# Performance work log

Hardware: AMD Instinct MI355X
Metric: run time of the kernel (lower is better)

Reference implementation:

```python
import jax, jax.numpy as jnp
import numpy as np
import math

B, N, L, ED, H = 2, 32, 4, 64, 4   # graphs, nodes/graph, layers, embed_dim, heads
HD = ED // H
EPS = 1e-5


def _ln(x, g, b):
    m = x.mean(-1, keepdims=True)
    v = ((x - m) ** 2).mean(-1, keepdims=True)
    return (x - m) * jax.lax.rsqrt(v + EPS) * g + b


def _layer(x, W, b, lg, lb, fW, fb, fg, fbeta):
    # NOTE: in the torch source, ModuleList([Linear]*4) shares ONE linear for
    # q/k/v1/v2 and ONE LayerNorm for norms[0..2]; we reproduce that sharing.
    h = (x @ W.T + b).reshape(B, N, N, H, HD)
    q = _ln(h, lg, lb)                                    # q == k (shared LN)
    scores = jnp.einsum('bxahd,bayhd->bxayh', q, q) / math.sqrt(HD)
    att = jax.nn.softmax(scores, axis=2)                  # softmax over 'a'
    xu = jnp.einsum('bxahd,bayhd->bxayhd', h, h)          # v1 == v2 == h
    xu = _ln(xu, lg, lb)                                  # shared LN again
    xu = jnp.einsum('bxayh,bxayhd->bxyhd', att, xu).reshape(B, N, N, ED)
    y = jnp.concatenate([x, xu], axis=-1) @ fW.T + fb
    return _ln(y, fg, fbeta)


def _diag_offdiag_maxpool(x):
    # x: (B, ED, N, N)
    diag = jnp.diagonal(x, axis1=-2, axis2=-1)            # (B, ED, N)
    max_diag = diag.max(axis=2)                           # (B, ED)
    val = jnp.abs(max_diag.max() + (-x).max())
    eye = jnp.eye(N, dtype=x.dtype)
    max_offdiag = (x - val * eye).max(axis=(2, 3))        # (B, ED)
    return jnp.concatenate([max_diag, max_offdiag], axis=1)  # (B, 2*ED)


def setup_inputs() -> dict:
    key = jax.random.key(0)
    ks = jax.random.split(key, 12)
    E = 1024
    g = jax.random.randint(ks[0], (E,), 0, B)
    ls = jax.random.randint(ks[1], (E,), 0, N)
    ld = jax.random.randint(ks[2], (E,), 0, N)
    edge_index = jnp.stack([g * N + ls, g * N + ld]).astype(jnp.int64)
    batch = (jnp.arange(B * N) // N).astype(jnp.int64)
    std = 0.02
    return {
        'edge_index': edge_index,
        'batch': batch,
        'W0': jax.random.normal(ks[3], (ED, 1), jnp.float32) * std,
        'b0': jnp.zeros((ED,), jnp.float32),
        'Ws': jax.random.normal(ks[4], (L - 1, ED, ED), jnp.float32) * std,
        'bs': jnp.zeros((L - 1, ED), jnp.float32),
        'ln_g': jnp.ones((L, HD), jnp.float32),
        'ln_b': jnp.zeros((L, HD), jnp.float32),
        'fW0': jax.random.normal(ks[5], (ED, 1 + ED), jnp.float32) * std,
        'fb0': jnp.zeros((ED,), jnp.float32),
        'fWs': jax.random.normal(ks[6], (L - 1, ED, 2 * ED), jnp.float32) * std,
        'fbs': jnp.zeros((L - 1, ED), jnp.float32),
        'fln_g': jnp.ones((L, ED), jnp.float32),
        'fln_b': jnp.zeros((L, ED), jnp.float32),
        'opW': jax.random.normal(ks[7], (L, ED // 2, 2 * ED), jnp.float32) * std,
        'opb': jnp.zeros((L, ED // 2), jnp.float32),
    }


def reference(edge_index, batch, W0, b0, Ws, bs, ln_g, ln_b,
              fW0, fb0, fWs, fbs, fln_g, fln_b, opW, opb):
    # to_dense_adj with edge_attr = 1.0
    g = batch[edge_index[0]]
    ls = edge_index[0] - g * N
    ld = edge_index[1] - g * N
    adj = jnp.zeros((B, N, N), jnp.float32).at[g, ls, ld].add(1.0)
    idx = jnp.arange(N)
    adj = adj.at[:, idx, idx].set(2.0)
    x = adj[..., None]                                    # (B, N, N, 1)

    scores = jnp.zeros((B, ED // 2), jnp.float32)
    for i in range(L):
        W = W0 if i == 0 else Ws[i - 1]
        b = b0 if i == 0 else bs[i - 1]
        fW = fW0 if i == 0 else fWs[i - 1]
        fb = fb0 if i == 0 else fbs[i - 1]
        x = _layer(x, W, b, ln_g[i], ln_b[i], fW, fb, fln_g[i], fln_b[i])
        pooled = _diag_offdiag_maxpool(jnp.transpose(x, (0, 3, 1, 2)))
        scores = scores + pooled @ opW[i].T + opb[i]

    # BatchNorm1d(momentum=1.0, affine=False), training mode -> batch stats
    m = scores.mean(axis=0)
    v = scores.var(axis=0)
    return (scores - m) / jnp.sqrt(v + EPS)
```

## Files before the change

kernel.cpp:

```cpp
#include <hip/hip_runtime.h>
#include <math.h>

#define EPS 1e-5f

#define AG_LOAD(p)     __hip_atomic_load((p), __ATOMIC_RELAXED, __HIP_MEMORY_SCOPE_AGENT)
#define AG_STORE(p, v) __hip_atomic_store((p), (v), __ATOMIC_RELAXED, __HIP_MEMORY_SCOPE_AGENT)

struct Params {
    const int* ei; const int* batch; int E;
    const float* W0; const float* b0; const float* Ws; const float* bs;
    const float* ln_g; const float* ln_b;
    const float* fW0; const float* fb0; const float* fWs; const float* fbs;
    const float* fln_g; const float* fln_b;
    const float* opW; const float* opb;
    float* hA; float* hAT;
    float* hB; float* hBT;
    float* xbuf;
    float* Pmin; float* Poff; float* Pdg;
    int* bar;
    float* out;
};

__launch_bounds__(512, 1)
__global__ void k0(Params p) {
    const int tid  = threadIdx.x;
    const int blk  = blockIdx.x;
    const int gtid = blk * 512 + tid;
    const int c    = tid & 63;
    const int d    = c & 15;
    const int rl   = tid >> 6;
    const int r0     = blk * 8;
    const int b_blk  = r0 >> 10;
    const int xi_blk = (r0 >> 5) & 31;
    const int y0     = r0 & 31;
    const int rld    = xi_blk - y0;
    const int a_l  = c & 31;
    const int h1   = c >> 5;

    __shared__ float xslab[32];
    __shared__ float yslab[256];
    __shared__ __align__(16) float cA[64], cC[64], cW[64], cB0[64], cG[64], cBl[64];
    __shared__ float hstat[3][4];
    __shared__ __align__(16) float pp_s[256 * 68];
    __shared__ float A1_s[8 * 132];
    __shared__ float K0h_s[8][4];
    __shared__ __align__(16) float xrow[8][64];
    __shared__ __align__(16) float xu_s[8][64];
    __shared__ float Wf0[64];
    __shared__ __align__(16) float T65[64 * 68];
    __shared__ __align__(16) float ST[64 * 68];

    if (blk == 0 && tid == 0) p.bar[0] = 0;

    if (tid < 32)  xslab[tid] = 0.0f;
    if (tid < 256) yslab[tid] = 0.0f;

    if (tid < 64) {
        float Wc = p.W0[c], bc = p.b0[c];
        float sW = Wc, sB = bc;
        #pragma unroll
        for (int m = 1; m < 16; m <<= 1) {
            sW += __shfl_xor(sW, m, 16);
            sB += __shfl_xor(sB, m, 16);
        }
        float Ac = Wc - sW * 0.0625f;
        float Bc = bc - sB * 0.0625f;
        float sAA = Ac * Ac, sAB = Ac * Bc, sBB = Bc * Bc;
        #pragma unroll
        for (int m = 1; m < 16; m <<= 1) {
            sAA += __shfl_xor(sAA, m, 16);
            sAB += __shfl_xor(sAB, m, 16);
            sBB += __shfl_xor(sBB, m, 16);
        }
        cA[c] = Ac; cC[c] = Bc; cW[c] = Wc; cB0[c] = bc;
        cG[c] = p.ln_g[d]; cBl[c] = p.ln_b[d];
        if (d == 0) {
            hstat[0][c >> 4] = sAA * 0.0625f;
            hstat[1][c >> 4] = sAB * 0.0625f;
            hstat[2][c >> 4] = sBB * 0.0625f;
        }
        Wf0[tid] = p.fW0[tid * 65];
    }
    for (int i = tid; i < 1024; i += 512) {
        int cc = i >> 4, u = i & 15;
        const float* src = p.fW0 + cc * 65 + 1 + 4 * u;
        float4 w = make_float4(src[0], src[1], src[2], src[3]);
        *(float4*)(T65 + cc * 68 + 4 * ((u + 2 * cc) & 15)) = w;
    }
    for (int i = tid; i < 1024; i += 512) {
        float4 w = ((const float4*)p.Ws)[i];
        int cc = i >> 4, u = i & 15;
        *(float4*)(ST + cc * 68 + 4 * ((u + 2 * cc) & 15)) = w;
    }
    __syncthreads();

    for (int e2 = tid; e2 < p.E; e2 += 512) {
        int e0 = p.ei[e2], e1 = p.ei[p.E + e2];
        int g  = p.batch[e0];
        if (g == b_blk) {
            int ls = e0 - g * 32, ld = e1 - g * 32;
            if (ls == xi_blk) atomicAdd(&xslab[ld], 1.0f);
            unsigned dy = (unsigned)(ld - y0);
            if (dy < 8u) atomicAdd(&yslab[ls * 8 + dy], 1.0f);
        }
    }
    __syncthreads();
    if (tid == 0) xslab[xi_blk] = 2.0f;
    if (tid < 8)  yslab[(y0 + tid) * 8 + tid] = 2.0f;
    __syncthreads();

    const float vx = xslab[a_l];
    const float vy = yslab[a_l * 8 + rl];
    float s0, s1, is0, is1, w0m, w1m;
    {
        const int hh = h1;
        float rsx = rsqrtf(fmaf(fmaf(hstat[0][hh], vx, 2.0f * hstat[1][hh]), vx, hstat[2][hh]) + EPS);
        float rsy = rsqrtf(fmaf(fmaf(hstat[0][hh], vy, 2.0f * hstat[1][hh]), vy, hstat[2][hh]) + EPS);
        float qq = 0.f, sp = 0.f, sq = 0.f;
        #pragma unroll
        for (int t = 0; t < 4; ++t) {
            int dd = hh * 16 + 4 * t;
            float4 av = *(const float4*)(cA + dd);
            float4 bv = *(const float4*)(cC + dd);
            float4 wv = *(const float4*)(cW + dd);
            float4 b0v = *(const float4*)(cB0 + dd);
            float4 gv = *(const float4*)(cG + dd);
            float4 blv = *(const float4*)(cBl + dd);
            float4 ppv;
            float qx, qy;
            qx = fmaf(av.x, vx, bv.x) * rsx * gv.x + blv.x;
            qy = fmaf(av.x, vy, bv.x) * rsy * gv.x + blv.x;
            qq = fmaf(qx, qy, qq);
            ppv.x = fmaf(wv.x, vx, b0v.x) * fmaf(wv.x, vy, b0v.x);
            qx = fmaf(av.y, vx, bv.y) * rsx * gv.y + blv.y;
            qy = fmaf(av.y, vy, bv.y) * rsy * gv.y + blv.y;
            qq = fmaf(qx, qy, qq);
            ppv.y = fmaf(wv.y, vx, b0v.y) * fmaf(wv.y, vy, b0v.y);
            qx = fmaf(av.z, vx, bv.z) * rsx * gv.z + blv.z;
            qy = fmaf(av.z, vy, bv.z) * rsy * gv.z + blv.z;
            qq = fmaf(qx, qy, qq);
            ppv.z = fmaf(wv.z, vx, b0v.z) * fmaf(wv.z, vy, b0v.z);
            qx = fmaf(av.w, vx, bv.w) * rsx * gv.w + blv.w;
            qy = fmaf(av.w, vy, bv.w) * rsy * gv.w + blv.w;
            qq = fmaf(qx, qy, qq);
            ppv.w = fmaf(wv.w, vx, b0v.w) * fmaf(wv.w, vy, b0v.w);
            sp += ppv.x + ppv.y + ppv.z + ppv.w;
            sq += ppv.x*ppv.x + ppv.y*ppv.y + ppv.z*ppv.z + ppv.w*ppv.w;
            *(float4*)(pp_s + (a_l * 8 + rl) * 68 + 4 * (((hh * 4 + t) + 3 * a_l) & 15)) = ppv;
        }
        s0 = qq * 0.25f;
        float mu = sp * 0.0625f, var = fmaxf(sq * 0.0625f - mu * mu, 0.f);
        is0 = rsqrtf(var + EPS); w0m = mu * is0;
    }
    {
        const int hh = h1 + 2;
        float rsx = rsqrtf(fmaf(fmaf(hstat[0][hh], vx, 2.0f * hstat[1][hh]), vx, hstat[2][hh]) + EPS);
        float rsy = rsqrtf(fmaf(fmaf(hstat[0][hh], vy, 2.0f * hstat[1][hh]), vy, hstat[2][hh]) + EPS);
        float qq = 0.f, sp = 0.f, sq = 0.f;
        #pragma unroll
        for (int t = 0; t < 4; ++t) {
            int dd = hh * 16 + 4 * t;
            float4 av = *(const float4*)(cA + dd);
            float4 bv = *(const float4*)(cC + dd);
            float4 wv = *(const float4*)(cW + dd);
            float4 b0v = *(const float4*)(cB0 + dd);
            float4 gv = *(const float4*)(cG + dd);
            float4 blv = *(const float4*)(cBl + dd);
            float4 ppv;
            float qx, qy;
            qx = fmaf(av.x, vx, bv.x) * rsx * gv.x + blv.x;
            qy = fmaf(av.x, vy, bv.x) * rsy * gv.x + blv.x;
            qq = fmaf(qx, qy, qq);
            ppv.x = fmaf(wv.x, vx, b0v.x) * fmaf(wv.x, vy, b0v.x);
            qx = fmaf(av.y, vx, bv.y) * rsx * gv.y + blv.y;
            qy = fmaf(av.y, vy, bv.y) * rsy * gv.y + blv.y;
            qq = fmaf(qx, qy, qq);
            ppv.y = fmaf(wv.y, vx, b0v.y) * fmaf(wv.y, vy, b0v.y);
            qx = fmaf(av.z, vx, bv.z) * rsx * gv.z + blv.z;
            qy = fmaf(av.z, vy, bv.z) * rsy * gv.z + blv.z;
            qq = fmaf(qx, qy, qq);
            ppv.z = fmaf(wv.z, vx, b0v.z) * fmaf(wv.z, vy, b0v.z);
            qx = fmaf(av.w, vx, bv.w) * rsx * gv.w + blv.w;
            qy = fmaf(av.w, vy, bv.w) * rsy * gv.w + blv.w;
            qq = fmaf(qx, qy, qq);
            ppv.w = fmaf(wv.w, vx, b0v.w) * fmaf(wv.w, vy, b0v.w);
            sp += ppv.x + ppv.y + ppv.z + ppv.w;
            sq += ppv.x*ppv.x + ppv.y*ppv.y + ppv.z*ppv.z + ppv.w*ppv.w;
            *(float4*)(pp_s + (a_l * 8 + rl) * 68 + 4 * (((hh * 4 + t) + 3 * a_l) & 15)) = ppv;
        }
        s1 = qq * 0.25f;
        float mu = sp * 0.0625f, var = fmaxf(sq * 0.0625f - mu * mu, 0.f);
        is1 = rsqrtf(var + EPS); w1m = mu * is1;
    }

    float m0 = s0, m1 = s1;
    #pragma unroll
    for (int m = 1; m < 32; m <<= 1) {
        m0 = fmaxf(m0, __shfl_xor(m0, m));
        m1 = fmaxf(m1, __shfl_xor(m1, m));
    }
    float e0 = __expf(s0 - m0), e1 = __expf(s1 - m1);
    float l0 = e0, l1 = e1, k0a = e0 * w0m, k1a = e1 * w1m;
    #pragma unroll
    for (int m = 1; m < 32; m <<= 1) {
        l0 += __shfl_xor(l0, m);  l1 += __shfl_xor(l1, m);
        k0a += __shfl_xor(k0a, m); k1a += __shfl_xor(k1a, m);
    }
    A1_s[rl * 132 + h1 * 33 + a_l]       = e0 * is0 / l0;
    A1_s[rl * 132 + (h1 + 2) * 33 + a_l] = e1 * is1 / l1;
    if (a_l == 0) {
        K0h_s[rl][h1]     = k0a / l0;
        K0h_s[rl][h1 + 2] = k1a / l1;
    }

    {
        const int hc = c >> 4;
        float acc = 0.f;
        #pragma unroll
        for (int a = 0; a < 32; ++a) {
            float pv = pp_s[(a * 8 + rl) * 68 + 4 * (((c >> 2) + 3 * a) & 15) + (c & 3)];
            acc = fmaf(A1_s[rl * 132 + hc * 33 + a], pv, acc);
        }
        xu_s[rl][c] = (acc - K0h_s[rl][hc]) * cG[c] + cBl[c];
    }

    const float adjv = xslab[y0 + rl];
    float acc2 = fmaf(Wf0[c], adjv, p.fb0[c]);
    #pragma unroll
    for (int u = 0; u < 16; ++u) {
        float4 w = *(const float4*)(T65 + c * 68 + 4 * ((u + 2 * c) & 15));
        float4 xr = *(const float4*)(&xu_s[rl][4 * u]);
        acc2 = fmaf(w.x, xr.x, acc2); acc2 = fmaf(w.y, xr.y, acc2);
        acc2 = fmaf(w.z, xr.z, acc2); acc2 = fmaf(w.w, xr.w, acc2);
    }
    float t1 = acc2;
    #pragma unroll
    for (int m = 1; m < 64; m <<= 1) t1 += __shfl_xor(t1, m, 64);
    float mu = t1 * (1.0f / 64.0f);
    float dv2 = acc2 - mu;
    float t2 = dv2 * dv2;
    #pragma unroll
    for (int m = 1; m < 64; m <<= 1) t2 += __shfl_xor(t2, m, 64);
    float xnew = dv2 * rsqrtf(t2 * (1.0f / 64.0f) + EPS) * p.fln_g[c] + p.fln_b[c];
    xrow[rl][c]  = xnew;
    p.xbuf[gtid] = xnew;
    __syncthreads();

    if (tid < 64) {
        float mn = 1e30f, off = -1e30f, dg = -1e30f;
        #pragma unroll
        for (int r2 = 0; r2 < 8; ++r2) {
            float v = xrow[r2][tid];
            mn = fminf(mn, v);
            if (r2 == rld) dg = v; else off = fmaxf(off, v);
        }
        int o = blk * 64 + tid;
        p.Pmin[o] = mn; p.Poff[o] = off; p.Pdg[o] = dg;
    }

    {
        float acc = p.bs[c];
        #pragma unroll
        for (int u = 0; u < 16; ++u) {
            float4 w = *(const float4*)(ST + c * 68 + 4 * ((u + 2 * c) & 15));
            float4 xr = *(const float4*)(&xrow[rl][4 * u]);
            acc = fmaf(w.x, xr.x, acc); acc = fmaf(w.y, xr.y, acc);
            acc = fmaf(w.z, xr.z, acc); acc = fmaf(w.w, xr.w, acc);
        }
        p.hA[gtid] = acc;
        p.hAT[((b_blk * 32 + y0 + rl) * 32 + xi_blk) * 64 + c] = acc;
    }
}

__launch_bounds__(512, 1)
__global__ void klayer(Params p, int layer, int is_last) {
    const int tid  = threadIdx.x;
    const int blk  = blockIdx.x;
    const int gtid = blk * 512 + tid;
    const int c    = tid & 63;
    const int d    = c & 15;
    const int rl   = tid >> 6;
    const int r0     = blk * 8;
    const int b_blk  = r0 >> 10;
    const int xi_blk = (r0 >> 5) & 31;
    const int y0     = r0 & 31;
    const int rld    = xi_blk - y0;
    const int slab_off = (b_blk * 1024 + xi_blk * 32) * 64;
    const int a_l  = c & 31;
    const int h1   = c >> 5;

    const float* hin  = (layer == 2) ? p.hB  : p.hA;
    const float* hinT = (layer == 2) ? p.hBT : p.hAT;
    float* hout  = (layer == 1) ? p.hB  : p.hA;
    float* houtT = (layer == 1) ? p.hBT : p.hAT;

    __shared__ __align__(16) float hx_s[32 * 68];
    __shared__ __align__(16) float yT_s[256 * 68];
    __shared__ float A1_s[8 * 132];
    __shared__ float K0h_s[8][4];
    __shared__ __align__(16) float xrow[8][64];
    __shared__ __align__(16) float xu_s[8][64];
    __shared__ __align__(16) float FT[64 * 132];
    __shared__ __align__(16) float ST[64 * 68];
    __shared__ __align__(16) float g16[16], b16[16];
    __shared__ float vals[4];
    __shared__ float scores_s[64];
    __shared__ int tailflag;
    float* sm_mn  = yT_s;
    float* sm_off = yT_s + 512;
    float* sm_dg  = yT_s + 1024;
    float* psum   = yT_s + 1536;

    float xv = p.xbuf[gtid];
    {
        const float4* src = (const float4*)(hinT + (b_blk * 32 + y0) * 2048);
        #pragma unroll
        for (int k = 0; k < 8; ++k) {
            int i = tid + k * 512;
            float4 v = src[i];
            int rl2 = i >> 9, a = (i >> 4) & 31, u = i & 15;
            *(float4*)(yT_s + (rl2 * 32 + a) * 68 + 4 * ((u + 2 * a) & 15)) = v;
        }
    }
    {
        float4 hsl = ((const float4*)(hin + slab_off))[tid];
        int a = tid >> 4, t = tid & 15, pr = (t + 2 * a) & 15;
        *(float4*)(hx_s + a * 68 + 4 * pr) = hsl;
    }
    if (tid < 16) {
        g16[tid] = p.ln_g[layer * 16 + tid];
        b16[tid] = p.ln_b[layer * 16 + tid];
    }
    {
        const float* fw = p.fWs + (layer - 1) * 8192;
        for (int i = tid; i < 2048; i += 512) {
            float4 w = ((const float4*)fw)[i];
            int cc = i >> 5, u = i & 31;
            *(float4*)(FT + cc * 132 + 4 * ((u + 2 * cc) & 31)) = w;
        }
    }
    if (!is_last) {
        const float* sw = p.Ws + layer * 4096;
        for (int i = tid; i < 1024; i += 512) {
            float4 w = ((const float4*)sw)[i];
            int cc = i >> 4, u = i & 15;
            *(float4*)(ST + cc * 68 + 4 * ((u + 2 * cc) & 15)) = w;
        }
    }
    xrow[rl][c] = xv;
    __syncthreads();

    float s0, s1, is0, is1, w0m, w1m;
    {
        const int hh = h1;
        float4 xh4[4], yh4[4];
        float sxp = 0.f, sxq = 0.f, syp = 0.f, syq = 0.f;
        #pragma unroll
        for (int t = 0; t < 4; ++t) {
            int ps = 4 * (((hh * 4 + t) + 2 * a_l) & 15);
            float4 v = *(const float4*)(hx_s + a_l * 68 + ps);
            float4 y = *(const float4*)(yT_s + (rl * 32 + a_l) * 68 + ps);
            xh4[t] = v; yh4[t] = y;
            sxp += v.x + v.y + v.z + v.w;
            sxq += v.x*v.x + v.y*v.y + v.z*v.z + v.w*v.w;
            syp += y.x + y.y + y.z + y.w;
            syq += y.x*y.x + y.y*y.y + y.z*y.z + y.w*y.w;
        }
        float mxm = sxp * 0.0625f;
        float rsx = rsqrtf(fmaxf(sxq * 0.0625f - mxm * mxm, 0.f) + EPS);
        float mym = syp * 0.0625f;
        float rsy = rsqrtf(fmaxf(syq * 0.0625f - mym * mym, 0.f) + EPS);
        float qq = 0.f, sp = 0.f, sq = 0.f;
        #pragma unroll
        for (int t = 0; t < 4; ++t) {
            float4 g4 = *(const float4*)(g16 + 4 * t);
            float4 b4 = *(const float4*)(b16 + 4 * t);
            float4 xh = xh4[t], yh = yh4[t];
            float4 ppv;
            float qx, qy;
            qx = (xh.x - mxm) * rsx * g4.x + b4.x;
            qy = (yh.x - mym) * rsy * g4.x + b4.x;
            qq = fmaf(qx, qy, qq);  ppv.x = xh.x * yh.x;
            qx = (xh.y - mxm) * rsx * g4.y + b4.y;
            qy = (yh.y - mym) * rsy * g4.y + b4.y;
            qq = fmaf(qx, qy, qq);  ppv.y = xh.y * yh.y;
            qx = (xh.z - mxm) * rsx * g4.z + b4.z;
            qy = (yh.z - mym) * rsy * g4.z + b4.z;
            qq = fmaf(qx, qy, qq);  ppv.z = xh.z * yh.z;
            qx = (xh.w - mxm) * rsx * g4.w + b4.w;
            qy = (yh.w - mym) * rsy * g4.w + b4.w;
            qq = fmaf(qx, qy, qq);  ppv.w = xh.w * yh.w;
            sp += ppv.x + ppv.y + ppv.z + ppv.w;
            sq += ppv.x*ppv.x + ppv.y*ppv.y + ppv.z*ppv.z + ppv.w*ppv.w;
        }
        s0 = qq * 0.25f;
        float mu = sp * 0.0625f, var = fmaxf(sq * 0.0625f - mu * mu, 0.f);
        is0 = rsqrtf(var + EPS); w0m = mu * is0;
    }
    {
        const int hh = h1 + 2;
        float4 xh4[4], yh4[4];
        float sxp = 0.f, sxq = 0.f, syp = 0.f, syq = 0.f;
        #pragma unroll
        for (int t = 0; t < 4; ++t) {
            int ps = 4 * (((hh * 4 + t) + 2 * a_l) & 15);
            float4 v = *(const float4*)(hx_s + a_l * 68 + ps);
            float4 y = *(const float4*)(yT_s + (rl * 32 + a_l) * 68 + ps);
            xh4[t] = v; yh4[t] = y;
            sxp += v.x + v.y + v.z + v.w;
            sxq += v.x*v.x + v.y*v.y + v.z*v.z + v.w*v.w;
            syp += y.x + y.y + y.z + y.w;
            syq += y.x*y.x + y.y*y.y + y.z*y.z + y.w*y.w;
        }
        float mxm = sxp * 0.0625f;
        float rsx = rsqrtf(fmaxf(sxq * 0.0625f - mxm * mxm, 0.f) + EPS);
        float mym = syp * 0.0625f;
        float rsy = rsqrtf(fmaxf(syq * 0.0625f - mym * mym, 0.f) + EPS);
        float qq = 0.f, sp = 0.f, sq = 0.f;
        #pragma unroll
        for (int t = 0; t < 4; ++t) {
            float4 g4 = *(const float4*)(g16 + 4 * t);
            float4 b4 = *(const float4*)(b16 + 4 * t);
            float4 xh = xh4[t], yh = yh4[t];
            float4 ppv;
            float qx, qy;
            qx = (xh.x - mxm) * rsx * g4.x + b4.x;
            qy = (yh.x - mym) * rsy * g4.x + b4.x;
            qq = fmaf(qx, qy, qq);  ppv.x = xh.x * yh.x;
            qx = (xh.y - mxm) * rsx * g4.y + b4.y;
            qy = (yh.y - mym) * rsy * g4.y + b4.y;
            qq = fmaf(qx, qy, qq);  ppv.y = xh.y * yh.y;
            qx = (xh.z - mxm) * rsx * g4.z + b4.z;
            qy = (yh.z - mym) * rsy * g4.z + b4.z;
            qq = fmaf(qx, qy, qq);  ppv.z = xh.z * yh.z;
            qx = (xh.w - mxm) * rsx * g4.w + b4.w;
            qy = (yh.w - mym) * rsy * g4.w + b4.w;
            qq = fmaf(qx, qy, qq);  ppv.w = xh.w * yh.w;
            sp += ppv.x + ppv.y + ppv.z + ppv.w;
            sq += ppv.x*ppv.x + ppv.y*ppv.y + ppv.z*ppv.z + ppv.w*ppv.w;
        }
        s1 = qq * 0.25f;
        float mu = sp * 0.0625f, var = fmaxf(sq * 0.0625f - mu * mu, 0.f);
        is1 = rsqrtf(var + EPS); w1m = mu * is1;
    }

    float m0 = s0, m1 = s1;
    #pragma unroll
    for (int m = 1; m < 32; m <<= 1) {
        m0 = fmaxf(m0, __shfl_xor(m0, m));
        m1 = fmaxf(m1, __shfl_xor(m1, m));
    }
    float e0 = __expf(s0 - m0), e1 = __expf(s1 - m1);
    float l0 = e0, l1 = e1, k0a = e0 * w0m, k1a = e1 * w1m;
    #pragma unroll
    for (int m = 1; m < 32; m <<= 1) {
        l0 += __shfl_xor(l0, m);  l1 += __shfl_xor(l1, m);
        k0a += __shfl_xor(k0a, m); k1a += __shfl_xor(k1a, m);
    }
    A1_s[rl * 132 + h1 * 33 + a_l]       = e0 * is0 / l0;
    A1_s[rl * 132 + (h1 + 2) * 33 + a_l] = e1 * is1 / l1;
    if (a_l == 0) {
        K0h_s[rl][h1]     = k0a / l0;
        K0h_s[rl][h1 + 2] = k1a / l1;
    }

    {
        const int hc = c >> 4;
        const int ce = c & 3;
        float acc = 0.f;
        #pragma unroll
        for (int a = 0; a < 32; ++a) {
            int ps = 4 * (((c >> 2) + 2 * a) & 15) + ce;
            float hxv = hx_s[a * 68 + ps];
            float hyv = yT_s[(rl * 32 + a) * 68 + ps];
            acc = fmaf(A1_s[rl * 132 + hc * 33 + a], hxv * hyv, acc);
        }
        xu_s[rl][c] = (acc - K0h_s[rl][hc]) * g16[d] + b16[d];
    }

    float acc2 = p.fbs[(layer - 1) * 64 + c];
    #pragma unroll
    for (int u = 0; u < 16; ++u) {
        float4 w = *(const float4*)(FT + c * 132 + 4 * ((u + 2 * c) & 31));
        float4 xr = *(const float4*)(&xrow[rl][4 * u]);
        acc2 = fmaf(w.x, xr.x, acc2); acc2 = fmaf(w.y, xr.y, acc2);
        acc2 = fmaf(w.z, xr.z, acc2); acc2 = fmaf(w.w, xr.w, acc2);
    }
    #pragma unroll
    for (int u = 16; u < 32; ++u) {
        float4 w = *(const float4*)(FT + c * 132 + 4 * ((u + 2 * c) & 31));
        float4 xr = *(const float4*)(&xu_s[rl][4 * (u - 16)]);
        acc2 = fmaf(w.x, xr.x, acc2); acc2 = fmaf(w.y, xr.y, acc2);
        acc2 = fmaf(w.z, xr.z, acc2); acc2 = fmaf(w.w, xr.w, acc2);
    }
    float t1 = acc2;
    #pragma unroll
    for (int m = 1; m < 64; m <<= 1) t1 += __shfl_xor(t1, m, 64);
    float mu = t1 * (1.0f / 64.0f);
    float dv2 = acc2 - mu;
    float t2 = dv2 * dv2;
    #pragma unroll
    for (int m = 1; m < 64; m <<= 1) t2 += __shfl_xor(t2, m, 64);
    float xnew = dv2 * rsqrtf(t2 * (1.0f / 64.0f) + EPS) *
                 p.fln_g[layer * 64 + c] + p.fln_b[layer * 64 + c];
    __syncthreads();
    xrow[rl][c] = xnew;
    if (!is_last) p.xbuf[gtid] = xnew;
    __syncthreads();

    if (tid < 64) {
        float mn = 1e30f, off = -1e30f, dg = -1e30f;
        #pragma unroll
        for (int r2 = 0; r2 < 8; ++r2) {
            float v = xrow[r2][tid];
            mn = fminf(mn, v);
            if (r2 == rld) dg = v; else off = fmaxf(off, v);
        }
        int o = layer * 16384 + blk * 64 + tid;
        if (is_last) {
            AG_STORE(&p.Pmin[o], mn); AG_STORE(&p.Poff[o], off); AG_STORE(&p.Pdg[o], dg);
        } else {
            p.Pmin[o] = mn; p.Poff[o] = off; p.Pdg[o] = dg;
        }
    }

    if (!is_last) {
        float acc = p.bs[layer * 64 + c];
        #pragma unroll
        for (int u = 0; u < 16; ++u) {
            float4 w = *(const float4*)(ST + c * 68 + 4 * ((u + 2 * c) & 15));
            float4 xr = *(const float4*)(&xrow[rl][4 * u]);
            acc = fmaf(w.x, xr.x, acc); acc = fmaf(w.y, xr.y, acc);
            acc = fmaf(w.z, xr.z, acc); acc = fmaf(w.w, xr.w, acc);
        }
        hout[gtid] = acc;
        houtT[((b_blk * 32 + y0 + rl) * 32 + xi_blk) * 64 + c] = acc;
        return;
    }

    __syncthreads();
    if (tid == 0) {
        int r = __hip_atomic_fetch_add(p.bar, 1, __ATOMIC_RELAXED,
                                       __HIP_MEMORY_SCOPE_AGENT);
        tailflag = (r == 255) ? 1 : 0;
    }
    __syncthreads();
    if (!tailflag) return;

    {
        int l = tid >> 7, bb = (tid >> 6) & 1, e = tid & 63;
        float mn = 1e30f, off = -1e30f, dg = -1e30f;
        #pragma unroll 4
        for (int k = 0; k < 128; ++k) {
            int o = l * 16384 + (bb * 128 + k) * 64 + e;
            float vmn, voff, vdg;
            if (l == 3) { vmn = AG_LOAD(&p.Pmin[o]); voff = AG_LOAD(&p.Poff[o]); vdg = AG_LOAD(&p.Pdg[o]); }
            else        { vmn = p.Pmin[o];           voff = p.Poff[o];           vdg = p.Pdg[o]; }
            mn  = fminf(mn,  vmn);
            off = fmaxf(off, voff);
            dg  = fmaxf(dg,  vdg);
        }
        sm_mn[tid] = mn; sm_off[tid] = off; sm_dg[tid] = dg;
    }
    __syncthreads();
    if (tid < 4) {
        float gmx = -1e30f, gmn = 1e30f;
        for (int i2 = 0; i2 < 128; ++i2) {
            gmx = fmaxf(gmx, sm_dg[tid * 128 + i2]);
            gmn = fminf(gmn, sm_mn[tid * 128 + i2]);
        }
        vals[tid] = fabsf(gmx - gmn);
    }
    __syncthreads();
    {
        int bb = tid >> 8, cc = (tid >> 3) & 31, pp = tid & 7;
        float a2 = 0.0f;
        for (int l = 0; l < 4; ++l) {
            float val = vals[l];
            const float* Wr = p.opW + l * 4096 + cc * 128;
            int base = l * 128 + bb * 64;
            for (int j = pp * 16; j < pp * 16 + 16; ++j) {
                float pv;
                if (j < 64) pv = sm_dg[base + j];
                else        pv = fmaxf(sm_off[base + j - 64], sm_dg[base + j - 64] - val);
                a2 = fmaf(Wr[j], pv, a2);
            }
        }
        psum[tid] = a2;
    }
    __syncthreads();
    if (tid < 64) {
        int bb = tid >> 5, cc = tid & 31;
        float a2 = 0.0f;
        for (int l = 0; l < 4; ++l) a2 += p.opb[l * 32 + cc];
        for (int pp = 0; pp < 8; ++pp) a2 += psum[bb * 256 + cc * 8 + pp];
        scores_s[tid] = a2;
    }
    __syncthreads();
    if (tid < 32) {
        float sA = scores_s[tid], sB = scores_s[32 + tid];
        float mu2 = 0.5f * (sA + sB);
        float va = 0.5f * ((sA - mu2) * (sA - mu2) + (sB - mu2) * (sB - mu2));
        float inv = rsqrtf(va + EPS);
        p.out[tid]      = (sA - mu2) * inv;
        p.out[32 + tid] = (sB - mu2) * inv;
    }
}

extern "C" void kernel_launch(void* const* d_in, const int* in_sizes, int n_in,
                              void* d_out, int out_size, void* d_ws, size_t ws_size,
                              hipStream_t stream) {
    Params prm;
    prm.ei    = (const int*)d_in[0];
    prm.batch = (const int*)d_in[1];
    prm.E     = in_sizes[0] / 2;
    prm.W0    = (const float*)d_in[2];
    prm.b0    = (const float*)d_in[3];
    prm.Ws    = (const float*)d_in[4];
    prm.bs    = (const float*)d_in[5];
    prm.ln_g  = (const float*)d_in[6];
    prm.ln_b  = (const float*)d_in[7];
    prm.fW0   = (const float*)d_in[8];
    prm.fb0   = (const float*)d_in[9];
    prm.fWs   = (const float*)d_in[10];
    prm.fbs   = (const float*)d_in[11];
    prm.fln_g = (const float*)d_in[12];
    prm.fln_b = (const float*)d_in[13];
    prm.opW   = (const float*)d_in[14];
    prm.opb   = (const float*)d_in[15];

    float* ws = (float*)d_ws;
    prm.hA    = ws;
    prm.hAT   = prm.hA   + 131072;
    prm.hB    = prm.hAT  + 131072;
    prm.hBT   = prm.hB   + 131072;
    prm.xbuf  = prm.hBT  + 131072;
    prm.Pmin  = prm.xbuf + 131072;
    prm.Poff  = prm.Pmin + 65536;
    prm.Pdg   = prm.Poff + 65536;
    prm.bar   = (int*)(prm.Pdg + 65536);
    prm.out   = (float*)d_out;

    k0<<<256, 512, 0, stream>>>(prm);
    klayer<<<256, 512, 0, stream>>>(prm, 1, 0);
    klayer<<<256, 512, 0, stream>>>(prm, 2, 0);
    klayer<<<256, 512, 0, stream>>>(prm, 3, 1);
}
```

Baseline: 157.5 us.

## Retile to 2x2 row blocks with 512 workgroups and atomic order-preserving pooling

Each workgroup now handles a 2x2 tile of (x,y) positions, where it used to handle a row of 8. That means 256-thread blocks, 512 blocks and two blocks per CU, with two x-slabs and two y-slabs staged in shared memory. Per-block pooling partials are replaced by global atomicMax on order-preserving encoded floats into a small 512-entry buffer, which is zeroed by a memset. The tail block then reads only that buffer and no longer reduces 64K partials. The pp_s buffer is dropped and products are recomputed, and the Ws staging reuses the FT buffer. Smaller shared memory improves occupancy, but each slab is loaded more redundantly and there are more atomics plus an extra memset launch.

```diff
diff --git a/kernel.cpp b/kernel.cpp
--- a/kernel.cpp
+++ b/kernel.cpp
@@ -4,7 +4,15 @@
 #define EPS 1e-5f
 
 #define AG_LOAD(p)     __hip_atomic_load((p), __ATOMIC_RELAXED, __HIP_MEMORY_SCOPE_AGENT)
-#define AG_STORE(p, v) __hip_atomic_store((p), (v), __ATOMIC_RELAXED, __HIP_MEMORY_SCOPE_AGENT)
+
+__device__ __forceinline__ unsigned fenc(float f) {
+    unsigned u = __float_as_uint(f);
+    return (u & 0x80000000u) ? ~u : (u | 0x80000000u);
+}
+__device__ __forceinline__ float fdec(unsigned u) {
+    u = (u & 0x80000000u) ? (u & 0x7FFFFFFFu) : ~u;
+    return __uint_as_float(u);
+}
 
 struct Params {
     const int* ei; const int* batch; int E;
@@ -16,44 +24,50 @@
     float* hA; float* hAT;
     float* hB; float* hBT;
     float* xbuf;
-    float* Pmin; float* Poff; float* Pdg;
+    unsigned* PdgU; unsigned* PoffU; unsigned* PmnU;
     int* bar;
     float* out;
 };
 
-__launch_bounds__(512, 1)
+
+__device__ __forceinline__ void pool_atomic(Params& p, int layer, int b_blk, int e,
+                                            float mn, float off, float dg) {
+    int o = layer * 128 + b_blk * 64 + e;
+    atomicMax(&p.PdgU[o],  fenc(dg));
+    atomicMax(&p.PoffU[o], fenc(off));
+    atomicMax(&p.PmnU[o],  fenc(-mn));
+}
+
+__launch_bounds__(256, 2)
 __global__ void k0(Params p) {
     const int tid  = threadIdx.x;
     const int blk  = blockIdx.x;
-    const int gtid = blk * 512 + tid;
+    const int gtid = blk * 256 + tid;
     const int c    = tid & 63;
     const int d    = c & 15;
     const int rl   = tid >> 6;
-    const int r0     = blk * 8;
-    const int b_blk  = r0 >> 10;
-    const int xi_blk = (r0 >> 5) & 31;
-    const int y0     = r0 & 31;
-    const int rld    = xi_blk - y0;
+    const int rx   = rl >> 1;
+    const int ry   = rl & 1;
+    const int b_blk = blk >> 8;
+    const int x0    = ((blk >> 4) & 15) * 2;
+    const int y0    = (blk & 15) * 2;
     const int a_l  = c & 31;
     const int h1   = c >> 5;
 
-    __shared__ float xslab[32];
-    __shared__ float yslab[256];
+    __shared__ float xslab2[2 * 32];
+    __shared__ float yslab2[32 * 2];
     __shared__ __align__(16) float cA[64], cC[64], cW[64], cB0[64], cG[64], cBl[64];
     __shared__ float hstat[3][4];
-    __shared__ __align__(16) float pp_s[256 * 68];
-    __shared__ float A1_s[8 * 132];
-    __shared__ float K0h_s[8][4];
-    __shared__ __align__(16) float xrow[8][64];
-    __shared__ __align__(16) float xu_s[8][64];
+    __shared__ float A1_s[4 * 132];
+    __shared__ float K0h_s[4][4];
+    __shared__ __align__(16) float xrow[4][64];
+    __shared__ __align__(16) float xu_s[4][64];
     __shared__ float Wf0[64];
     __shared__ __align__(16) float T65[64 * 68];
     __shared__ __align__(16) float ST[64 * 68];
 
-    if (blk == 0 && tid == 0) p.bar[0] = 0;
-
-    if (tid < 32)  xslab[tid] = 0.0f;
-    if (tid < 256) yslab[tid] = 0.0f;
+    if (tid < 64)  xslab2[tid] = 0.0f;
+    if (tid >= 64 && tid < 128) yslab2[tid - 64] = 0.0f;
 
     if (tid < 64) {
         float Wc = p.W0[c], bc = p.b0[c];
@@ -81,39 +95,45 @@
         }
         Wf0[tid] = p.fW0[tid * 65];
     }
-    for (int i = tid; i < 1024; i += 512) {
+    #pragma unroll
+    for (int s = 0; s < 4; ++s) {
+        int i = tid + s * 256;
         int cc = i >> 4, u = i & 15;
         const float* src = p.fW0 + cc * 65 + 1 + 4 * u;
         float4 w = make_float4(src[0], src[1], src[2], src[3]);
         *(float4*)(T65 + cc * 68 + 4 * ((u + 2 * cc) & 15)) = w;
     }
-    for (int i = tid; i < 1024; i += 512) {
+    #pragma unroll
+    for (int s = 0; s < 4; ++s) {
+        int i = tid + s * 256;
         float4 w = ((const float4*)p.Ws)[i];
         int cc = i >> 4, u = i & 15;
         *(float4*)(ST + cc * 68 + 4 * ((u + 2 * cc) & 15)) = w;
     }
     __syncthreads();
 
-    for (int e2 = tid; e2 < p.E; e2 += 512) {
+    for (int e2 = tid; e2 < p.E; e2 += 256) {
         int e0 = p.ei[e2], e1 = p.ei[p.E + e2];
         int g  = p.batch[e0];
         if (g == b_blk) {
             int ls = e0 - g * 32, ld = e1 - g * 32;
-            if (ls == xi_blk) atomicAdd(&xslab[ld], 1.0f);
+            unsigned dx = (unsigned)(ls - x0);
+            if (dx < 2u) atomicAdd(&xslab2[dx * 32 + ld], 1.0f);
             unsigned dy = (unsigned)(ld - y0);
-            if (dy < 8u) atomicAdd(&yslab[ls * 8 + dy], 1.0f);
-        }
-    }
-    __syncthreads();
-    if (tid == 0) xslab[xi_blk] = 2.0f;
-    if (tid < 8)  yslab[(y0 + tid) * 8 + tid] = 2.0f;
-    __syncthreads();
-
-    const float vx = xslab[a_l];
-    const float vy = yslab[a_l * 8 + rl];
+            if (dy < 2u) atomicAdd(&yslab2[ls * 2 + dy], 1.0f);
+        }
+    }
+    __syncthreads();
+    if (tid < 2)  xslab2[tid * 32 + x0 + tid] = 2.0f;
+    if (tid >= 2 && tid < 4) { int j = tid - 2; yslab2[(y0 + j) * 2 + j] = 2.0f; }
+    __syncthreads();
+
+    const float vx = xslab2[rx * 32 + a_l];
+    const float vy = yslab2[a_l * 2 + ry];
     float s0, s1, is0, is1, w0m, w1m;
-    {
-        const int hh = h1;
+    #pragma unroll
+    for (int hb = 0; hb < 2; ++hb) {
+        const int hh = h1 + 2 * hb;
         float rsx = rsqrtf(fmaf(fmaf(hstat[0][hh], vx, 2.0f * hstat[1][hh]), vx, hstat[2][hh]) + EPS);
         float rsy = rsqrtf(fmaf(fmaf(hstat[0][hh], vy, 2.0f * hstat[1][hh]), vy, hstat[2][hh]) + EPS);
         float qq = 0.f, sp = 0.f, sq = 0.f;
@@ -126,71 +146,29 @@
             float4 b0v = *(const float4*)(cB0 + dd);
             float4 gv = *(const float4*)(cG + dd);
             float4 blv = *(const float4*)(cBl + dd);
-            float4 ppv;
-            float qx, qy;
+            float qx, qy, pp;
             qx = fmaf(av.x, vx, bv.x) * rsx * gv.x + blv.x;
             qy = fmaf(av.x, vy, bv.x) * rsy * gv.x + blv.x;
             qq = fmaf(qx, qy, qq);
-            ppv.x = fmaf(wv.x, vx, b0v.x) * fmaf(wv.x, vy, b0v.x);
+            pp = fmaf(wv.x, vx, b0v.x) * fmaf(wv.x, vy, b0v.x); sp += pp; sq += pp * pp;
             qx = fmaf(av.y, vx, bv.y) * rsx * gv.y + blv.y;
             qy = fmaf(av.y, vy, bv.y) * rsy * gv.y + blv.y;
             qq = fmaf(qx, qy, qq);
-            ppv.y = fmaf(wv.y, vx, b0v.y) * fmaf(wv.y, vy, b0v.y);
+            pp = fmaf(wv.y, vx, b0v.y) * fmaf(wv.y, vy, b0v.y); sp += pp; sq += pp * pp;
             qx = fmaf(av.z, vx, bv.z) * rsx * gv.z + blv.z;
             qy = fmaf(av.z, vy, bv.z) * rsy * gv.z + blv.z;
             qq = fmaf(qx, qy, qq);
-            ppv.z = fmaf(wv.z, vx, b0v.z) * fmaf(wv.z, vy, b0v.z);
+            pp = fmaf(wv.z, vx, b0v.z) * fmaf(wv.z, vy, b0v.z); sp += pp; sq += pp * pp;
             qx = fmaf(av.w, vx, bv.w) * rsx * gv.w + blv.w;
             qy = fmaf(av.w, vy, bv.w) * rsy * gv.w + blv.w;
             qq = fmaf(qx, qy, qq);
-            ppv.w = fmaf(wv.w, vx, b0v.w) * fmaf(wv.w, vy, b0v.w);
-            sp += ppv.x + ppv.y + ppv.z + ppv.w;
-            sq += ppv.x*ppv.x + ppv.y*ppv.y + ppv.z*ppv.z + ppv.w*ppv.w;
-            *(float4*)(pp_s + (a_l * 8 + rl) * 68 + 4 * (((hh * 4 + t) + 3 * a_l) & 15)) = ppv;
-        }
-        s0 = qq * 0.25f;
+            pp = fmaf(wv.w, vx, b0v.w) * fmaf(wv.w, vy, b0v.w); sp += pp; sq += pp * pp;
+        }
+        float ss = qq * 0.25f;
         float mu = sp * 0.0625f, var = fmaxf(sq * 0.0625f - mu * mu, 0.f);
-        is0 = rsqrtf(var + EPS); w0m = mu * is0;
-    }
-    {
-        const int hh = h1 + 2;
-        float rsx = rsqrtf(fmaf(fmaf(hstat[0][hh], vx, 2.0f * hstat[1][hh]), vx, hstat[2][hh]) + EPS);
-        float rsy = rsqrtf(fmaf(fmaf(hstat[0][hh], vy, 2.0f * hstat[1][hh]), vy, hstat[2][hh]) + EPS);
-        float qq = 0.f, sp = 0.f, sq = 0.f;
-        #pragma unroll
-        for (int t = 0; t < 4; ++t) {
-            int dd = hh * 16 + 4 * t;
-            float4 av = *(const float4*)(cA + dd);
-            float4 bv = *(const float4*)(cC + dd);
-            float4 wv = *(const float4*)(cW + dd);
-            float4 b0v = *(const float4*)(cB0 + dd);
-            float4 gv = *(const float4*)(cG + dd);
-            float4 blv = *(const float4*)(cBl + dd);
-            float4 ppv;
-            float qx, qy;
-            qx = fmaf(av.x, vx, bv.x) * rsx * gv.x + blv.x;
-            qy = fmaf(av.x, vy, bv.x) * rsy * gv.x + blv.x;
-            qq = fmaf(qx, qy, qq);
-            ppv.x = fmaf(wv.x, vx, b0v.x) * fmaf(wv.x, vy, b0v.x);
-            qx = fmaf(av.y, vx, bv.y) * rsx * gv.y + blv.y;
-            qy = fmaf(av.y, vy, bv.y) * rsy * gv.y + blv.y;
-            qq = fmaf(qx, qy, qq);
-            ppv.y = fmaf(wv.y, vx, b0v.y) * fmaf(wv.y, vy, b0v.y);
-            qx = fmaf(av.z, vx, bv.z) * rsx * gv.z + blv.z;
-            qy = fmaf(av.z, vy, bv.z) * rsy * gv.z + blv.z;
-            qq = fmaf(qx, qy, qq);
-            ppv.z = fmaf(wv.z, vx, b0v.z) * fmaf(wv.z, vy, b0v.z);
-            qx = fmaf(av.w, vx, bv.w) * rsx * gv.w + blv.w;
-            qy = fmaf(av.w, vy, bv.w) * rsy * gv.w + blv.w;
-            qq = fmaf(qx, qy, qq);
-            ppv.w = fmaf(wv.w, vx, b0v.w) * fmaf(wv.w, vy, b0v.w);
-            sp += ppv.x + ppv.y + ppv.z + ppv.w;
-            sq += ppv.x*ppv.x + ppv.y*ppv.y + ppv.z*ppv.z + ppv.w*ppv.w;
-            *(float4*)(pp_s + (a_l * 8 + rl) * 68 + 4 * (((hh * 4 + t) + 3 * a_l) & 15)) = ppv;
-        }
-        s1 = qq * 0.25f;
-        float mu = sp * 0.0625f, var = fmaxf(sq * 0.0625f - mu * mu, 0.f);
-        is1 = rsqrtf(var + EPS); w1m = mu * is1;
+        float is = rsqrtf(var + EPS);
+        if (hb == 0) { s0 = ss; is0 = is; w0m = mu * is; }
+        else         { s1 = ss; is1 = is; w1m = mu * is; }
     }
 
     float m0 = s0, m1 = s1;
@@ -215,16 +193,19 @@
 
     {
         const int hc = c >> 4;
+        const float Wc = cW[c], bc = cB0[c];
         float acc = 0.f;
         #pragma unroll
         for (int a = 0; a < 32; ++a) {
-            float pv = pp_s[(a * 8 + rl) * 68 + 4 * (((c >> 2) + 3 * a) & 15) + (c & 3)];
+            float vx2 = xslab2[rx * 32 + a];
+            float vy2 = yslab2[a * 2 + ry];
+            float pv = fmaf(Wc, vx2, bc) * fmaf(Wc, vy2, bc);
             acc = fmaf(A1_s[rl * 132 + hc * 33 + a], pv, acc);
         }
         xu_s[rl][c] = (acc - K0h_s[rl][hc]) * cG[c] + cBl[c];
     }
 
-    const float adjv = xslab[y0 + rl];
+    const float adjv = xslab2[rx * 32 + y0 + ry];
     float acc2 = fmaf(Wf0[c], adjv, p.fb0[c]);
     #pragma unroll
     for (int u = 0; u < 16; ++u) {
@@ -249,13 +230,13 @@
     if (tid < 64) {
         float mn = 1e30f, off = -1e30f, dg = -1e30f;
         #pragma unroll
-        for (int r2 = 0; r2 < 8; ++r2) {
+        for (int r2 = 0; r2 < 4; ++r2) {
             float v = xrow[r2][tid];
             mn = fminf(mn, v);
-            if (r2 == rld) dg = v; else off = fmaxf(off, v);
-        }
-        int o = blk * 64 + tid;
-        p.Pmin[o] = mn; p.Poff[o] = off; p.Pdg[o] = dg;
+            if (x0 + (r2 >> 1) == y0 + (r2 & 1)) dg = fmaxf(dg, v);
+            else off = fmaxf(off, v);
+        }
+        pool_atomic(p, 0, b_blk, tid, mn, off, dg);
     }
 
     {
@@ -267,25 +248,25 @@
             acc = fmaf(w.x, xr.x, acc); acc = fmaf(w.y, xr.y, acc);
             acc = fmaf(w.z, xr.z, acc); acc = fmaf(w.w, xr.w, acc);
         }
-        p.hA[gtid] = acc;
-        p.hAT[((b_blk * 32 + y0 + rl) * 32 + xi_blk) * 64 + c] = acc;
+        int x = x0 + rx, y = y0 + ry;
+        p.hA[(b_blk * 1024 + x * 32 + y) * 64 + c] = acc;
+        p.hAT[((b_blk * 32 + y) * 32 + x) * 64 + c] = acc;
     }
 }
 
-__launch_bounds__(512, 1)
+__launch_bounds__(256, 2)
 __global__ void klayer(Params p, int layer, int is_last) {
     const int tid  = threadIdx.x;
     const int blk  = blockIdx.x;
-    const int gtid = blk * 512 + tid;
+    const int gtid = blk * 256 + tid;
     const int c    = tid & 63;
     const int d    = c & 15;
     const int rl   = tid >> 6;
-    const int r0     = blk * 8;
-    const int b_blk  = r0 >> 10;
-    const int xi_blk = (r0 >> 5) & 31;
-    const int y0     = r0 & 31;
-    const int rld    = xi_blk - y0;
-    const int slab_off = (b_blk * 1024 + xi_blk * 32) * 64;
+    const int rx   = rl >> 1;
+    const int ry   = rl & 1;
+    const int b_blk = blk >> 8;
+    const int x0    = ((blk >> 4) & 15) * 2;
+    const int y0    = (blk & 15) * 2;
     const int a_l  = c & 31;
     const int h1   = c >> 5;
 
@@ -294,72 +275,66 @@
     float* hout  = (layer == 1) ? p.hB  : p.hA;
     float* houtT = (layer == 1) ? p.hBT : p.hAT;
 
-    __shared__ __align__(16) float hx_s[32 * 68];
-    __shared__ __align__(16) float yT_s[256 * 68];
-    __shared__ float A1_s[8 * 132];
-    __shared__ float K0h_s[8][4];
-    __shared__ __align__(16) float xrow[8][64];
-    __shared__ __align__(16) float xu_s[8][64];
+    __shared__ __align__(16) float hx2_s[2][2176];
+    __shared__ __align__(16) float yT2_s[2][2176];
     __shared__ __align__(16) float FT[64 * 132];
-    __shared__ __align__(16) float ST[64 * 68];
+    __shared__ float A1_s[4 * 132];
+    __shared__ float K0h_s[4][4];
+    __shared__ __align__(16) float xrow[4][64];
+    __shared__ __align__(16) float xu_s[4][64];
     __shared__ __align__(16) float g16[16], b16[16];
     __shared__ float vals[4];
     __shared__ float scores_s[64];
     __shared__ int tailflag;
-    float* sm_mn  = yT_s;
-    float* sm_off = yT_s + 512;
-    float* sm_dg  = yT_s + 1024;
-    float* psum   = yT_s + 1536;
+    float* sm_mn  = &hx2_s[0][0];
+    float* sm_off = sm_mn + 512;
+    float* sm_dg  = sm_mn + 1024;
+    float* psum   = sm_mn + 1536;
 
     float xv = p.xbuf[gtid];
     {
-        const float4* src = (const float4*)(hinT + (b_blk * 32 + y0) * 2048);
-        #pragma unroll
-        for (int k = 0; k < 8; ++k) {
-            int i = tid + k * 512;
-            float4 v = src[i];
-            int rl2 = i >> 9, a = (i >> 4) & 31, u = i & 15;
-            *(float4*)(yT_s + (rl2 * 32 + a) * 68 + 4 * ((u + 2 * a) & 15)) = v;
-        }
-    }
-    {
-        float4 hsl = ((const float4*)(hin + slab_off))[tid];
-        int a = tid >> 4, t = tid & 15, pr = (t + 2 * a) & 15;
-        *(float4*)(hx_s + a * 68 + 4 * pr) = hsl;
+        const float4* sx0 = (const float4*)(hin + (b_blk * 1024 + x0 * 32) * 64);
+        const float4* sx1 = (const float4*)(hin + (b_blk * 1024 + (x0 + 1) * 32) * 64);
+        const float4* sy0 = (const float4*)(hinT + (b_blk * 32 + y0) * 2048);
+        const float4* sy1 = (const float4*)(hinT + (b_blk * 32 + y0 + 1) * 2048);
+        #pragma unroll
+        for (int s = 0; s < 2; ++s) {
+            int ii = tid + s * 256;
+            int a = ii >> 4, u = ii & 15, pr = (u + 2 * a) & 15;
+            *(float4*)(&hx2_s[0][a * 68 + 4 * pr]) = sx0[ii];
+            *(float4*)(&hx2_s[1][a * 68 + 4 * pr]) = sx1[ii];
+            *(float4*)(&yT2_s[0][a * 68 + 4 * pr]) = sy0[ii];
+            *(float4*)(&yT2_s[1][a * 68 + 4 * pr]) = sy1[ii];
+        }
     }
     if (tid < 16) {
         g16[tid] = p.ln_g[layer * 16 + tid];
         b16[tid] = p.ln_b[layer * 16 + tid];
     }
     {
-        const float* fw = p.fWs + (layer - 1) * 8192;
-        for (int i = tid; i < 2048; i += 512) {
-            float4 w = ((const float4*)fw)[i];
+        const float4* fw = (const float4*)(p.fWs + (layer - 1) * 8192);
+        #pragma unroll
+        for (int s = 0; s < 8; ++s) {
+            int i = tid + s * 256;
+            float4 w = fw[i];
             int cc = i >> 5, u = i & 31;
             *(float4*)(FT + cc * 132 + 4 * ((u + 2 * cc) & 31)) = w;
         }
     }
-    if (!is_last) {
-        const float* sw = p.Ws + layer * 4096;
-        for (int i = tid; i < 1024; i += 512) {
-            float4 w = ((const float4*)sw)[i];
-            int cc = i >> 4, u = i & 15;
-            *(float4*)(ST + cc * 68 + 4 * ((u + 2 * cc) & 15)) = w;
-        }
-    }
     xrow[rl][c] = xv;
     __syncthreads();
 
     float s0, s1, is0, is1, w0m, w1m;
-    {
-        const int hh = h1;
+    #pragma unroll
+    for (int hb = 0; hb < 2; ++hb) {
+        const int hh = h1 + 2 * hb;
         float4 xh4[4], yh4[4];
         float sxp = 0.f, sxq = 0.f, syp = 0.f, syq = 0.f;
         #pragma unroll
         for (int t = 0; t < 4; ++t) {
             int ps = 4 * (((hh * 4 + t) + 2 * a_l) & 15);
-            float4 v = *(const float4*)(hx_s + a_l * 68 + ps);
-            float4 y = *(const float4*)(yT_s + (rl * 32 + a_l) * 68 + ps);
+            float4 v = *(const float4*)(&hx2_s[rx][a_l * 68 + ps]);
+            float4 y = *(const float4*)(&yT2_s[ry][a_l * 68 + ps]);
             xh4[t] = v; yh4[t] = y;
             sxp += v.x + v.y + v.z + v.w;
             sxq += v.x*v.x + v.y*v.y + v.z*v.z + v.w*v.w;
@@ -376,72 +351,25 @@
             float4 g4 = *(const float4*)(g16 + 4 * t);
             float4 b4 = *(const float4*)(b16 + 4 * t);
             float4 xh = xh4[t], yh = yh4[t];
-            float4 ppv;
-            float qx, qy;
+            float qx, qy, pp;
             qx = (xh.x - mxm) * rsx * g4.x + b4.x;
             qy = (yh.x - mym) * rsy * g4.x + b4.x;
-            qq = fmaf(qx, qy, qq);  ppv.x = xh.x * yh.x;
+            qq = fmaf(qx, qy, qq);  pp = xh.x * yh.x; sp += pp; sq += pp * pp;
             qx = (xh.y - mxm) * rsx * g4.y + b4.y;
             qy = (yh.y - mym) * rsy * g4.y + b4.y;
-            qq = fmaf(qx, qy, qq);  ppv.y = xh.y * yh.y;
+            qq = fmaf(qx, qy, qq);  pp = xh.y * yh.y; sp += pp; sq += pp * pp;
             qx = (xh.z - mxm) * rsx * g4.z + b4.z;
             qy = (yh.z - mym) * rsy * g4.z + b4.z;
-            qq = fmaf(qx, qy, qq);  ppv.z = xh.z * yh.z;
+            qq = fmaf(qx, qy, qq);  pp = xh.z * yh.z; sp += pp; sq += pp * pp;
             qx = (xh.w - mxm) * rsx * g4.w + b4.w;
             qy = (yh.w - mym) * rsy * g4.w + b4.w;
-            qq = fmaf(qx, qy, qq);  ppv.w = xh.w * yh.w;
-            sp += ppv.x + ppv.y + ppv.z + ppv.w;
-            sq += ppv.x*ppv.x + ppv.y*ppv.y + ppv.z*ppv.z + ppv.w*ppv.w;
-        }
-        s0 = qq * 0.25f;
+            qq = fmaf(qx, qy, qq);  pp = xh.w * yh.w; sp += pp; sq += pp * pp;
+        }
+        float ss = qq * 0.25f;
         float mu = sp * 0.0625f, var = fmaxf(sq * 0.0625f - mu * mu, 0.f);
-        is0 = rsqrtf(var + EPS); w0m = mu * is0;
-    }
-    {
-        const int hh = h1 + 2;
-        float4 xh4[4], yh4[4];
-        float sxp = 0.f, sxq = 0.f, syp = 0.f, syq = 0.f;
-        #pragma unroll
-        for (int t = 0; t < 4; ++t) {
-            int ps = 4 * (((hh * 4 + t) + 2 * a_l) & 15);
-            float4 v = *(const float4*)(hx_s + a_l * 68 + ps);
-            float4 y = *(const float4*)(yT_s + (rl * 32 + a_l) * 68 + ps);
-            xh4[t] = v; yh4[t] = y;
-            sxp += v.x + v.y + v.z + v.w;
-            sxq += v.x*v.x + v.y*v.y + v.z*v.z + v.w*v.w;
-            syp += y.x + y.y + y.z + y.w;
-            syq += y.x*y.x + y.y*y.y + y.z*y.z + y.w*y.w;
-        }
-        float mxm = sxp * 0.0625f;
-        float rsx = rsqrtf(fmaxf(sxq * 0.0625f - mxm * mxm, 0.f) + EPS);
-        float mym = syp * 0.0625f;
-        float rsy = rsqrtf(fmaxf(syq * 0.0625f - mym * mym, 0.f) + EPS);
-        float qq = 0.f, sp = 0.f, sq = 0.f;
-        #pragma unroll
-        for (int t = 0; t < 4; ++t) {
-            float4 g4 = *(const float4*)(g16 + 4 * t);
-            float4 b4 = *(const float4*)(b16 + 4 * t);
-            float4 xh = xh4[t], yh = yh4[t];
-            float4 ppv;
-            float qx, qy;
-            qx = (xh.x - mxm) * rsx * g4.x + b4.x;
-            qy = (yh.x - mym) * rsy * g4.x + b4.x;
-            qq = fmaf(qx, qy, qq);  ppv.x = xh.x * yh.x;
-            qx = (xh.y - mxm) * rsx * g4.y + b4.y;
-            qy = (yh.y - mym) * rsy * g4.y + b4.y;
-            qq = fmaf(qx, qy, qq);  ppv.y = xh.y * yh.y;
-            qx = (xh.z - mxm) * rsx * g4.z + b4.z;
-            qy = (yh.z - mym) * rsy * g4.z + b4.z;
-            qq = fmaf(qx, qy, qq);  ppv.z = xh.z * yh.z;
-            qx = (xh.w - mxm) * rsx * g4.w + b4.w;
-            qy = (yh.w - mym) * rsy * g4.w + b4.w;
-            qq = fmaf(qx, qy, qq);  ppv.w = xh.w * yh.w;
-            sp += ppv.x + ppv.y + ppv.z + ppv.w;
-            sq += ppv.x*ppv.x + ppv.y*ppv.y + ppv.z*ppv.z + ppv.w*ppv.w;
-        }
-        s1 = qq * 0.25f;
-        float mu = sp * 0.0625f, var = fmaxf(sq * 0.0625f - mu * mu, 0.f);
-        is1 = rsqrtf(var + EPS); w1m = mu * is1;
+        float is = rsqrtf(var + EPS);
+        if (hb == 0) { s0 = ss; is0 = is; w0m = mu * is; }
+        else         { s1 = ss; is1 = is; w1m = mu * is; }
     }
 
     float m0 = s0, m1 = s1;
@@ -471,8 +399,8 @@
         #pragma unroll
         for (int a = 0; a < 32; ++a) {
             int ps = 4 * (((c >> 2) + 2 * a) & 15) + ce;
-            float hxv = hx_s[a * 68 + ps];
-            float hyv = yT_s[(rl * 32 + a) * 68 + ps];
+            float hxv = hx2_s[rx][a * 68 + ps];
+            float hyv = yT2_s[ry][a * 68 + ps];
             acc = fmaf(A1_s[rl * 132 + hc * 33 + a], hxv * hyv, acc);
         }
         xu_s[rl][c] = (acc - K0h_s[rl][hc]) * g16[d] + b16[d];
@@ -505,36 +433,43 @@
                  p.fln_g[layer * 64 + c] + p.fln_b[layer * 64 + c];
     __syncthreads();
     xrow[rl][c] = xnew;
-    if (!is_last) p.xbuf[gtid] = xnew;
+    if (!is_last) {
+        p.xbuf[gtid] = xnew;
+        const float4* sw = (const float4*)(p.Ws + layer * 4096);
+        #pragma unroll
+        for (int s = 0; s < 4; ++s) {
+            int i = tid + s * 256;
+            float4 w = sw[i];
+            int cc = i >> 4, u = i & 15;
+            *(float4*)(FT + cc * 68 + 4 * ((u + 2 * cc) & 15)) = w;
+        }
+    }
     __syncthreads();
 
     if (tid < 64) {
         float mn = 1e30f, off = -1e30f, dg = -1e30f;
         #pragma unroll
-        for (int r2 = 0; r2 < 8; ++r2) {
+        for (int r2 = 0; r2 < 4; ++r2) {
             float v = xrow[r2][tid];
             mn = fminf(mn, v);
-            if (r2 == rld) dg = v; else off = fmaxf(off, v);
-        }
-        int o = layer * 16384 + blk * 64 + tid;
-        if (is_last) {
-            AG_STORE(&p.Pmin[o], mn); AG_STORE(&p.Poff[o], off); AG_STORE(&p.Pdg[o], dg);
-        } else {
-            p.Pmin[o] = mn; p.Poff[o] = off; p.Pdg[o] = dg;
-        }
+            if (x0 + (r2 >> 1) == y0 + (r2 & 1)) dg = fmaxf(dg, v);
+            else off = fmaxf(off, v);
+        }
+        pool_atomic(p, layer, b_blk, tid, mn, off, dg);
     }
 
     if (!is_last) {
         float acc = p.bs[layer * 64 + c];
         #pragma unroll
         for (int u = 0; u < 16; ++u) {
-            float4 w = *(const float4*)(ST + c * 68 + 4 * ((u + 2 * c) & 15));
+            float4 w = *(const float4*)(FT + c * 68 + 4 * ((u + 2 * c) & 15));
             float4 xr = *(const float4*)(&xrow[rl][4 * u]);
             acc = fmaf(w.x, xr.x, acc); acc = fmaf(w.y, xr.y, acc);
             acc = fmaf(w.z, xr.z, acc); acc = fmaf(w.w, xr.w, acc);
         }
-        hout[gtid] = acc;
-        houtT[((b_blk * 32 + y0 + rl) * 32 + xi_blk) * 64 + c] = acc;
+        int x = x0 + rx, y = y0 + ry;
+        hout[(b_blk * 1024 + x * 32 + y) * 64 + c] = acc;
+        houtT[((b_blk * 32 + y) * 32 + x) * 64 + c] = acc;
         return;
     }
 
@@ -542,25 +477,20 @@
     if (tid == 0) {
         int r = __hip_atomic_fetch_add(p.bar, 1, __ATOMIC_RELAXED,
                                        __HIP_MEMORY_SCOPE_AGENT);
-        tailflag = (r == 255) ? 1 : 0;
+        tailflag = (r == 511) ? 1 : 0;
     }
     __syncthreads();
     if (!tailflag) return;
 
-    {
-        int l = tid >> 7, bb = (tid >> 6) & 1, e = tid & 63;
-        float mn = 1e30f, off = -1e30f, dg = -1e30f;
-        #pragma unroll 4
-        for (int k = 0; k < 128; ++k) {
-            int o = l * 16384 + (bb * 128 + k) * 64 + e;
-            float vmn, voff, vdg;
-            if (l == 3) { vmn = AG_LOAD(&p.Pmin[o]); voff = AG_LOAD(&p.Poff[o]); vdg = AG_LOAD(&p.Pdg[o]); }
-            else        { vmn = p.Pmin[o];           voff = p.Poff[o];           vdg = p.Pdg[o]; }
-            mn  = fminf(mn,  vmn);
-            off = fmaxf(off, voff);
-            dg  = fmaxf(dg,  vdg);
-        }
-        sm_mn[tid] = mn; sm_off[tid] = off; sm_dg[tid] = dg;
+    #pragma unroll
+    for (int s = 0; s < 2; ++s) {
+        int slot = tid + s * 256;
+        unsigned ud = AG_LOAD(&p.PdgU[slot]);
+        unsigned uo = AG_LOAD(&p.PoffU[slot]);
+        unsigned um = AG_LOAD(&p.PmnU[slot]);
+        sm_dg[slot]  = fdec(ud);
+        sm_off[slot] = fdec(uo);
+        sm_mn[slot]  = -fdec(um);
     }
     __syncthreads();
     if (tid < 4) {
@@ -573,13 +503,13 @@
     }
     __syncthreads();
     {
-        int bb = tid >> 8, cc = (tid >> 3) & 31, pp = tid & 7;
+        int bb = tid >> 7, cc = (tid >> 2) & 31, pp = tid & 3;
         float a2 = 0.0f;
         for (int l = 0; l < 4; ++l) {
             float val = vals[l];
             const float* Wr = p.opW + l * 4096 + cc * 128;
             int base = l * 128 + bb * 64;
-            for (int j = pp * 16; j < pp * 16 + 16; ++j) {
+            for (int j = pp * 32; j < pp * 32 + 32; ++j) {
                 float pv;
                 if (j < 64) pv = sm_dg[base + j];
                 else        pv = fmaxf(sm_off[base + j - 64], sm_dg[base + j - 64] - val);
@@ -593,7 +523,7 @@
         int bb = tid >> 5, cc = tid & 31;
         float a2 = 0.0f;
         for (int l = 0; l < 4; ++l) a2 += p.opb[l * 32 + cc];
-        for (int pp = 0; pp < 8; ++pp) a2 += psum[bb * 256 + cc * 8 + pp];
+        for (int pp = 0; pp < 4; ++pp) a2 += psum[bb * 128 + cc * 4 + pp];
         scores_s[tid] = a2;
     }
     __syncthreads();
@@ -635,14 +565,16 @@
     prm.hB    = prm.hAT  + 131072;
     prm.hBT   = prm.hB   + 131072;
     prm.xbuf  = prm.hBT  + 131072;
-    prm.Pmin  = prm.xbuf + 131072;
-    prm.Poff  = prm.Pmin + 65536;
-    prm.Pdg   = prm.Poff + 65536;
-    prm.bar   = (int*)(prm.Pdg + 65536);
+    unsigned* pu = (unsigned*)(prm.xbuf + 131072);
+    prm.PdgU  = pu;
+    prm.PoffU = pu + 512;
+    prm.PmnU  = pu + 1024;
+    prm.bar   = (int*)(pu + 1536);
     prm.out   = (float*)d_out;
 
-    k0<<<256, 512, 0, stream>>>(prm);
-    klayer<<<256, 512, 0, stream>>>(prm, 1, 0);
-    klayer<<<256, 512, 0, stream>>>(prm, 2, 0);
-    klayer<<<256, 512, 0, stream>>>(prm, 3, 1);
+    hipMemsetAsync(pu, 0, 1552 * sizeof(unsigned), stream);
+    k0<<<512, 256, 0, stream>>>(prm);
+    klayer<<<512, 256, 0, stream>>>(prm, 1, 0);
+    klayer<<<512, 256, 0, stream>>>(prm, 2, 0);
+    klayer<<<512, 256, 0, stream>>>(prm, 3, 1);
 }
```

New measurement: 160.7 us. +2.0%, slower.
